# Kernel optimization log

Hardware: AMD Instinct MI355X
Metric: run time of the kernel (lower is better)

Reference implementation:

```python
import jax, jax.numpy as jnp
import numpy as np

T, N, E = 4, 20000, 320000
F_IN, EH, NH, GH, OUT = 12, 32, 64, 64, 1
NUM_LAYERS = 2
EB_IN = (EH + 2 * NH) * 2 + GH  # 384
NB_IN = 2 * NH + 2 * EH + GH    # 256
GB_IN = NH + EH + GH            # 160


def setup_inputs() -> dict:
    key = jax.random.key(0)
    ks = jax.random.split(key, 24)
    f32 = jnp.float32
    def w(k, fan_in, shape):
        return jax.random.normal(k, shape, f32) * (1.0 / np.sqrt(fan_in))
    return {
        "node_attr": jax.random.normal(ks[0], (T, N, F_IN), f32),
        "edge_attr": jax.random.normal(ks[1], (T, E, 1), f32),
        "edge_index": jax.random.randint(ks[2], (2, E), 0, N, jnp.int32),
        "sp_L_vals": jax.random.normal(ks[3], (E,), f32),
        "global_attr": jax.random.normal(ks[4], (1, GH), f32),
        "coeff": jnp.full((1,), 0.1, f32),
        "W_ee": w(ks[5], 1, (1, EH)), "b_ee": jnp.zeros((EH,), f32),
        "W_ne": w(ks[6], F_IN, (F_IN, NH)), "b_ne": jnp.zeros((NH,), f32),
        "W_eb": w(ks[7], EB_IN, (EB_IN, EH)), "b_eb": jnp.zeros((EH,), f32),
        "W_nb": w(ks[8], NB_IN, (NB_IN, NH)), "b_nb": jnp.zeros((NH,), f32),
        "W_gb": w(ks[9], GB_IN, (GB_IN, GH)), "b_gb": jnp.zeros((GH,), f32),
        "W_nd1": w(ks[10], NH, (NH, NH)), "b_nd1": jnp.zeros((NH,), f32),
        "W_nd2": w(ks[11], NH, (NH, OUT)), "b_nd2": jnp.zeros((OUT,), f32),
    }


def _forward(node_attr, edge_attr, edge_index, sp_L_vals, global_attr, coeff,
             W_ee, b_ee, W_ne, b_ne, W_eb, b_eb, W_nb, b_nb, W_gb, b_gb,
             W_nd1, b_nd1, W_nd2, b_nd2):
    relu = jax.nn.relu
    s, r = edge_index[0], edge_index[1]
    seg = lambda v, idx: jax.ops.segment_sum(v, idx, num_segments=N)
    c = coeff[0]

    # encoders
    x_enc = relu(node_attr @ W_ne + b_ne)   # [T,N,NH]
    e_enc = relu(edge_attr @ W_ee + b_ee)   # [T,E,EH]

    def run_gn(xT, eT, g0):
        # recurrent GN core over processing steps; hidden (h_x,h_e,h_g) starts at zeros
        def step(carry, inp):
            h_x, h_e, h_g = carry
            x_in, e_in = inp
            gE = jnp.broadcast_to(h_g, (E, GH))
            # EdgeBlock: [edge_in, edge_h, sender_in, sender_h, recv_in, recv_h, global]
            edge_cat = jnp.concatenate(
                [e_in, h_e, x_in[s], h_x[s], x_in[r], h_x[r], gE], axis=-1)
            e_new = relu(edge_cat @ W_eb + b_eb)              # [E,EH]
            sent = seg(e_new, s)                              # scatter_add by sender
            recv = seg(e_new, r)                              # scatter_add by receiver
            gN = jnp.broadcast_to(h_g, (N, GH))
            node_cat = jnp.concatenate([x_in, h_x, sent, recv, gN], axis=-1)
            x_new = relu(node_cat @ W_nb + b_nb)              # [N,NH]
            # GlobalBlock: scatter_mean == plain mean (single graph)
            g_cat = jnp.concatenate(
                [x_new.mean(0, keepdims=True), e_new.mean(0, keepdims=True), h_g], axis=-1)
            g_new = relu(g_cat @ W_gb + b_gb)                 # [1,GH]
            # physics terms (pde='diff'): time derivative = state update,
            # spatial derivative = coeff * (graph-Laplacian action via sp_L edge weights)
            t_der = x_new - h_x
            s_der = c * seg(sp_L_vals[:, None] * (x_new[s] - x_new[r]), r)
            return (x_new, e_new, g_new), (x_new, e_new, g_new, t_der, s_der)
        carry0 = (jnp.zeros((N, NH), jnp.float32), jnp.zeros((E, EH), jnp.float32), g0)
        _, ys = jax.lax.scan(step, carry0, (xT, eT))
        return ys  # xs[T,N,NH], es[T,E,EH], gs[T,1,GH], td[T,N,NH], sd[T,N,NH]

    xs, es, gs, td, sd = run_gn(x_enc, e_enc, global_attr)
    x_pre = x_enc
    for _ in range(NUM_LAYERS - 1):
        x_res = xs + x_pre          # residual node state feeds next GN layer
        x_pre = x_res
        xs, es, gs, td, sd = run_gn(x_res, es, gs[0])

    x_final = xs + x_pre            # add_residual=True final residual
    h = relu(x_final @ W_nd1 + b_nd1)
    out_nodes = h @ W_nd2 + b_nd2   # [T,N,OUT]
    return out_nodes, td, sd


def reference(node_attr, edge_attr, edge_index, sp_L_vals, global_attr, coeff,
              W_ee, b_ee, W_ne, b_ne, W_eb, b_eb, W_nb, b_nb, W_gb, b_gb,
              W_nd1, b_nd1, W_nd2, b_nd2):
    return _forward(node_attr, edge_attr, edge_index, sp_L_vals, global_attr, coeff,
                    W_ee, b_ee, W_ne, b_ne, W_eb, b_eb, W_nb, b_nb, W_gb, b_gb,
                    W_nd1, b_nd1, W_nd2, b_nd2)
```

## Files before the change

kernel.cpp:

```cpp
#include <hip/hip_runtime.h>


typedef __attribute__((ext_vector_type(8))) short s16x8;
typedef __attribute__((ext_vector_type(4))) float f32x4;

#define T_STEPS 4
#define NN 20000
#define NP 20224
#define NE 320000

__device__ __forceinline__ float bf2f(unsigned short h){
  return __uint_as_float(((unsigned)h)<<16);
}
__device__ __forceinline__ unsigned short f2bf(float f){
  unsigned u = __float_as_uint(f);
  return (unsigned short)((u + 0x7fffu + ((u>>16)&1u)) >> 16);
}
__device__ __forceinline__ float loadIn(const void* p, size_t i, int bf){
  return bf ? bf2f(((const unsigned short*)p)[i]) : ((const float*)p)[i];
}
__device__ __forceinline__ void storeOut(void* o, size_t i, float v, int bf){
  if(bf) ((unsigned short*)o)[i] = f2bf(v);
  else   ((float*)o)[i] = v;
}
__device__ __forceinline__ void load8(const float* __restrict__ p, float* v){
  const float4* q4 = (const float4*)p;
  float4 a = q4[0], b = q4[1];
  v[0]=a.x; v[1]=a.y; v[2]=a.z; v[3]=a.w;
  v[4]=b.x; v[5]=b.y; v[6]=b.z; v[7]=b.w;
}
__device__ __forceinline__ int4 pack8(const float* v){
  unsigned p0 = (unsigned)f2bf(v[0]) | ((unsigned)f2bf(v[1])<<16);
  unsigned p1 = (unsigned)f2bf(v[2]) | ((unsigned)f2bf(v[3])<<16);
  unsigned p2 = (unsigned)f2bf(v[4]) | ((unsigned)f2bf(v[5])<<16);
  unsigned p3 = (unsigned)f2bf(v[6]) | ((unsigned)f2bf(v[7])<<16);
  return make_int4((int)p0,(int)p1,(int)p2,(int)p3);
}
__device__ __forceinline__ void unp8(int4 w, float* a){
  unsigned x;
  x=(unsigned)w.x; a[0]=__uint_as_float(x<<16); a[1]=__uint_as_float(x&0xffff0000u);
  x=(unsigned)w.y; a[2]=__uint_as_float(x<<16); a[3]=__uint_as_float(x&0xffff0000u);
  x=(unsigned)w.z; a[4]=__uint_as_float(x<<16); a[5]=__uint_as_float(x&0xffff0000u);
  x=(unsigned)w.w; a[6]=__uint_as_float(x<<16); a[7]=__uint_as_float(x&0xffff0000u);
}

union I4S8 { int4 i; s16x8 s; };

struct ConvJob { const void* src; float* dst; int n; };
struct ConvJobs { ConvJob j[16]; int cnt; };

__global__ void conv_kernel(ConvJobs jobs, const void* coeff_in, int* flagp,
                            float* coeff_f, float* z, int zn){
  unsigned short u = ((const unsigned short*)coeff_in)[0];
  float as_bf = bf2f(u);
  int bf = (fabsf(as_bf - 0.1f) < 0.02f) ? 1 : 0;
  int tid = blockIdx.x*blockDim.x + threadIdx.x;
  if(tid==0){ *flagp = bf; *coeff_f = bf ? as_bf : ((const float*)coeff_in)[0]; }
  int stride = gridDim.x*blockDim.x;
  for(int q=0;q<jobs.cnt;q++){
    const void* s = jobs.j[q].src; float* d = jobs.j[q].dst; int n = jobs.j[q].n;
    for(int i=tid;i<n;i+=stride) d[i] = loadIn(s, i, bf);
  }
  for(int i=tid;i<zn;i+=stride) z[i]=0.f;
}

__global__ void csr_hist(const int* __restrict__ ei, int* deg_s, int* deg_r,
                         unsigned short* __restrict__ rank_s,
                         unsigned short* __restrict__ rank_r){
  int e = blockIdx.x*256+threadIdx.x;
  rank_s[e] = (unsigned short)atomicAdd(&deg_s[ei[e]],1);
  rank_r[e] = (unsigned short)atomicAdd(&deg_r[ei[NE+e]],1);
}

__global__ void csr_scan(const int* __restrict__ deg_s, int* __restrict__ off_s,
                         const int* __restrict__ deg_r, int* __restrict__ off_r){
  const int CH = NP/256;
  const int* deg = blockIdx.x ? deg_r : deg_s;
  int* off = blockIdx.x ? off_r : off_s;
  int t = threadIdx.x;
  int base = t*CH;
  int s = 0;
  #pragma unroll 8
  for(int i=0;i<CH;i++) s += deg[base+i];
  int lane = t & 63, w = t >> 6;
  int x = s;
  #pragma unroll
  for(int o=1;o<64;o<<=1){
    int y = __shfl_up(x, o, 64);
    if(lane >= o) x += y;
  }
  __shared__ int wtot[4];
  if(lane==63) wtot[w] = x;
  __syncthreads();
  int wbase = 0;
  #pragma unroll
  for(int k=0;k<3;k++) if(k<w) wbase += wtot[k];
  int acc = wbase + x - s;
  #pragma unroll 8
  for(int i=0;i<CH;i++){
    off[base+i]=acc; acc+=deg[base+i];
  }
  if(t==255) off[NN]=acc;
}

__global__ void fill_pack_enc_kernel(
  const int* __restrict__ ei,
  const int* __restrict__ s_off, const int* __restrict__ r_off,
  const unsigned short* __restrict__ rank_s,
  const unsigned short* __restrict__ rank_r,
  int* __restrict__ csr_s, int* __restrict__ csr_r, int2* __restrict__ sr2,
  const void* __restrict__ spL, float* __restrict__ spL_p,
  const void* __restrict__ W_eb_in, const void* __restrict__ W_nb_in,
  const void* __restrict__ W_nd1_in,
  unsigned short* __restrict__ WpE, unsigned short* __restrict__ WpN,
  unsigned short* __restrict__ WpD,
  const void* __restrict__ na, const float* __restrict__ W_ne,
  const float* __restrict__ b_ne, unsigned short* __restrict__ xA,
  const int* flagp)
{
  __shared__ float arow[4][12];
  const int blk = blockIdx.x;
  const int bf = *flagp;
  if(blk < NE/256){
    int e = blk*256+threadIdx.x;
    int s = ei[e], r = ei[NE+e];
    int p = r_off[r] + rank_r[e];
    sr2[p] = make_int2(s,r);
    csr_r[p] = e;
    csr_s[s_off[s]+rank_s[e]] = p;
    spL_p[p] = loadIn(spL, e, bf);
  } else if(blk < NE/256 + 128){
    int idx = (blk - NE/256)*256 + threadIdx.x;
    const void* W; unsigned short* P; int KW, NT;
    if(idx < 12288){ W=W_eb_in; P=WpE; KW=12; NT=2; }
    else if(idx < 28672){ idx -= 12288; W=W_nb_in; P=WpN; KW=8; NT=4; }
    else { idx -= 28672; W=W_nd1_in; P=WpD; KW=2; NT=4; }
    int j = idx & 7;
    int lane = (idx>>3) & 63;
    int rest = idx >> 9;
    int kw = rest % KW;
    int nt = rest / KW;
    int k = kw*32 + (lane>>4)*8 + j;
    int n = nt*16 + (lane&15);
    P[idx] = f2bf(loadIn(W, (size_t)k*(NT*16) + n, bf));
  } else {
    int lane = threadIdx.x & 63, nl = threadIdx.x >> 6;
    int row = (blk - (NE/256 + 128))*4 + nl;
    if(lane<12) arow[nl][lane] = loadIn(na, (size_t)row*12+lane, bf);
    __syncthreads();
    float acc = b_ne[lane];
    #pragma unroll
    for(int k=0;k<12;k++) acc += arow[nl][k]*W_ne[k*64+lane];
    xA[(size_t)row*64+lane] = f2bf(fmaxf(acc,0.f));
  }
}

__global__ __launch_bounds__(256,4) void edge_block_mfma(
  const int2* __restrict__ sr2,
  const unsigned short* __restrict__ x_in,
  const unsigned short* __restrict__ h_x,
  const void* __restrict__ e_attr,
  int e_attr_off,
  const int* __restrict__ inv,
  const unsigned short* __restrict__ e_in,
  const unsigned short* __restrict__ h_e,
  const float* __restrict__ g,
  const float* __restrict__ W_ee, const float* __restrict__ b_ee,
  const unsigned short* __restrict__ Wp,
  const float* __restrict__ b_eb,
  unsigned short* __restrict__ e_out,
  float* __restrict__ partial_e,
  const int* flagp)
{
  const int tid = threadIdx.x;
  const int lane = tid&63;
  const int q = lane>>4, m16 = lane&15;
  const int pair = blockIdx.x*4 + (tid>>6);
  const int e0 = pair*32;
  const int eg0 = e0 + m16, eg1 = e0 + 16 + m16;
  const int2 sr0 = sr2[eg0], sr1 = sr2[eg1];
  const int o8 = q*8;
  const int4 z4 = make_int4(0,0,0,0);

  I4S8 A0[12], A1[12];
  if(e_attr){
    int bf = *flagp;
    float a0v = loadIn(e_attr, (size_t)e_attr_off + inv[eg0], bf);
    float a1v = loadIn(e_attr, (size_t)e_attr_off + inv[eg1], bf);
    float v[8];
    #pragma unroll
    for(int j=0;j<8;j++) v[j] = fmaxf(a0v*W_ee[o8+j]+b_ee[o8+j], 0.f);
    A0[0].i = pack8(v);
    #pragma unroll
    for(int j=0;j<8;j++) v[j] = fmaxf(a1v*W_ee[o8+j]+b_ee[o8+j], 0.f);
    A1[0].i = pack8(v);
  } else {
    A0[0].i = ((const int4*)(e_in + (size_t)eg0*32))[q];
    A1[0].i = ((const int4*)(e_in + (size_t)eg1*32))[q];
  }
  A0[1].i = h_e ? ((const int4*)(h_e + (size_t)eg0*32))[q] : z4;
  A1[1].i = h_e ? ((const int4*)(h_e + (size_t)eg1*32))[q] : z4;
  { const int4* p0 = (const int4*)(x_in + (size_t)sr0.x*64);
    const int4* p1 = (const int4*)(x_in + (size_t)sr1.x*64);
    A0[2].i = p0[q]; A1[2].i = p1[q];
    A0[3].i = p0[4+q]; A1[3].i = p1[4+q]; }
  if(h_x){
    const int4* p0 = (const int4*)(h_x + (size_t)sr0.x*64);
    const int4* p1 = (const int4*)(h_x + (size_t)sr1.x*64);
    A0[4].i = p0[q]; A1[4].i = p1[q];
    A0[5].i = p0[4+q]; A1[5].i = p1[4+q];
  } else { A0[4].i=z4; A1[4].i=z4; A0[5].i=z4; A1[5].i=z4; }
  { const int4* p0 = (const int4*)(x_in + (size_t)sr0.y*64);
    const int4* p1 = (const int4*)(x_in + (size_t)sr1.y*64);
    A0[6].i = p0[q]; A1[6].i = p1[q];
    A0[7].i = p0[4+q]; A1[7].i = p1[4+q]; }
  if(h_x){
    const int4* p0 = (const int4*)(h_x + (size_t)sr0.y*64);
    const int4* p1 = (const int4*)(h_x + (size_t)sr1.y*64);
    A0[8].i = p0[q]; A1[8].i = p1[q];
    A0[9].i = p0[4+q]; A1[9].i = p1[4+q];
  } else { A0[8].i=z4; A1[8].i=z4; A0[9].i=z4; A1[9].i=z4; }
  { float v[8];
    load8(g + o8, v);      A0[10].i = pack8(v); A1[10].i = A0[10].i;
    load8(g + 32 + o8, v); A0[11].i = pack8(v); A1[11].i = A0[11].i; }

  f32x4 a00={0.f,0.f,0.f,0.f}, a01={0.f,0.f,0.f,0.f};
  f32x4 a10={0.f,0.f,0.f,0.f}, a11={0.f,0.f,0.f,0.f};
  #pragma unroll
  for(int kw=0;kw<12;kw++){
    s16x8 b0 = *(const s16x8*)(Wp + (size_t)(kw*64 + lane)*8);
    s16x8 b1 = *(const s16x8*)(Wp + (size_t)((12+kw)*64 + lane)*8);
    a00 = __builtin_amdgcn_mfma_f32_16x16x32_bf16(A0[kw].s, b0, a00, 0,0,0);
    a01 = __builtin_amdgcn_mfma_f32_16x16x32_bf16(A0[kw].s, b1, a01, 0,0,0);
    a10 = __builtin_amdgcn_mfma_f32_16x16x32_bf16(A1[kw].s, b0, a10, 0,0,0);
    a11 = __builtin_amdgcn_mfma_f32_16x16x32_bf16(A1[kw].s, b1, a11, 0,0,0);
  }

  float pe0=0.f, pe1=0.f;
  const float bb0 = b_eb[m16], bb1 = b_eb[16+m16];
  #pragma unroll
  for(int r=0;r<4;r++){
    int eg0m = e0 + q*4 + r;
    int eg1m = eg0m + 16;
    float v00 = fmaxf(a00[r]+bb0, 0.f);
    float v01 = fmaxf(a01[r]+bb1, 0.f);
    float v10 = fmaxf(a10[r]+bb0, 0.f);
    float v11 = fmaxf(a11[r]+bb1, 0.f);
    e_out[(size_t)eg0m*32+m16]    = f2bf(v00);
    e_out[(size_t)eg0m*32+16+m16] = f2bf(v01);
    e_out[(size_t)eg1m*32+m16]    = f2bf(v10);
    e_out[(size_t)eg1m*32+16+m16] = f2bf(v11);
    pe0 += v00+v10; pe1 += v01+v11;
  }
  pe0 += __shfl_xor(pe0,16,64); pe0 += __shfl_xor(pe0,32,64);
  pe1 += __shfl_xor(pe1,16,64); pe1 += __shfl_xor(pe1,32,64);
  if(q==0){
    int slot = blockIdx.x & 63;
    atomicAdd(&partial_e[slot*32+m16],    pe0);
    atomicAdd(&partial_e[slot*32+16+m16], pe1);
  }
}

__global__ void aggregate_kernel(const unsigned short* __restrict__ e_new,
  const int* __restrict__ s_off, const int* __restrict__ csr_s,
  const int* __restrict__ r_off,
  unsigned short* __restrict__ sentB, unsigned short* __restrict__ recvB)
{
  int node = blockIdx.x*4 + (threadIdx.x>>6);
  int lane = threadIdx.x & 63;
  int c4 = (lane & 7) * 4;
  int jr = lane >> 3;
  float s0=0.f,s1=0.f,s2=0.f,s3=0.f;
  float r0=0.f,r1=0.f,r2=0.f,r3=0.f;
  {
    int beg = s_off[node], end = s_off[node+1];
    for(int i=beg+jr; i<end; i+=8){
      uint2 w = *(const uint2*)(e_new + (size_t)csr_s[i]*32 + c4);
      s0 += __uint_as_float(w.x<<16);
      s1 += __uint_as_float(w.x&0xffff0000u);
      s2 += __uint_as_float(w.y<<16);
      s3 += __uint_as_float(w.y&0xffff0000u);
    }
  }
  {
    int beg = r_off[node], end = r_off[node+1];
    for(int i=beg+jr; i<end; i+=8){
      uint2 w = *(const uint2*)(e_new + (size_t)i*32 + c4);
      r0 += __uint_as_float(w.x<<16);
      r1 += __uint_as_float(w.x&0xffff0000u);
      r2 += __uint_as_float(w.y<<16);
      r3 += __uint_as_float(w.y&0xffff0000u);
    }
  }
  #pragma unroll
  for(int o=8;o<64;o<<=1){
    s0 += __shfl_xor(s0,o,64); s1 += __shfl_xor(s1,o,64);
    s2 += __shfl_xor(s2,o,64); s3 += __shfl_xor(s3,o,64);
    r0 += __shfl_xor(r0,o,64); r1 += __shfl_xor(r1,o,64);
    r2 += __shfl_xor(r2,o,64); r3 += __shfl_xor(r3,o,64);
  }
  if(jr==0){
    unsigned slo = (unsigned)f2bf(s0) | ((unsigned)f2bf(s1)<<16);
    unsigned shi = (unsigned)f2bf(s2) | ((unsigned)f2bf(s3)<<16);
    unsigned rlo = (unsigned)f2bf(r0) | ((unsigned)f2bf(r1)<<16);
    unsigned rhi = (unsigned)f2bf(r2) | ((unsigned)f2bf(r3)<<16);
    *(uint2*)(sentB + (size_t)node*32 + c4) = make_uint2(slo,shi);
    *(uint2*)(recvB + (size_t)node*32 + c4) = make_uint2(rlo,rhi);
  }
}

__global__ __launch_bounds__(256) void node_block_mfma(
  const unsigned short* __restrict__ x_in, const unsigned short* __restrict__ h_x,
  const unsigned short* __restrict__ sentB, const unsigned short* __restrict__ recvB,
  const float* __restrict__ g,
  const unsigned short* __restrict__ Wp,
  const float* __restrict__ b_nb,
  unsigned short* __restrict__ x_out,
  unsigned short* __restrict__ xres_out,
  float* __restrict__ partial_x,
  void* __restrict__ out_base, size_t td_off, int has_td,
  float* __restrict__ partial_e,
  const float* __restrict__ W_gb, const float* __restrict__ b_gb,
  float* __restrict__ g_out, int* __restrict__ cnt,
  const int* flagp)
{
  __shared__ int lastFlag;
  __shared__ float gcat[160];
  __shared__ float red[4][64];
  const int tid = threadIdx.x, lane = tid&63;
  const int q = lane>>4, m16 = lane&15;
  const int tile = blockIdx.x*4 + (tid>>6);
  if(tile < NN/16){
    const int n0 = tile*16;
    const int ng = n0+m16;
    const int o8 = q*8;
    const int4 z4 = make_int4(0,0,0,0);

    I4S8 A[8];
    { const int4* xp = (const int4*)(x_in + (size_t)ng*64);
      A[0].i = xp[q]; A[1].i = xp[4+q]; }
    if(h_x){ const int4* hp = (const int4*)(h_x + (size_t)ng*64);
      A[2].i = hp[q]; A[3].i = hp[4+q];
    } else { A[2].i = z4; A[3].i = z4; }
    A[4].i = ((const int4*)(sentB + (size_t)ng*32))[q];
    A[5].i = ((const int4*)(recvB + (size_t)ng*32))[q];
    { float v[8];
      load8(g + o8, v);      A[6].i = pack8(v);
      load8(g + 32 + o8, v); A[7].i = pack8(v); }

    f32x4 acc[4];
    #pragma unroll
    for(int nt=0;nt<4;nt++) acc[nt] = (f32x4){0.f,0.f,0.f,0.f};
    #pragma unroll
    for(int kw=0;kw<8;kw++){
      #pragma unroll
      for(int nt=0;nt<4;nt++){
        s16x8 b = *(const s16x8*)(Wp + (size_t)((nt*8+kw)*64 + lane)*8);
        acc[nt] = __builtin_amdgcn_mfma_f32_16x16x32_bf16(A[kw].s, b, acc[nt], 0,0,0);
      }
    }

    int bf = has_td ? *flagp : 0;
    float ps[4] = {0.f,0.f,0.f,0.f};
    #pragma unroll
    for(int r=0;r<4;r++){
      int nodeg = n0 + q*4 + r;
      #pragma unroll
      for(int nt=0;nt<4;nt++){
        int col = nt*16 + m16;
        float vv = fmaxf(acc[nt][r] + b_nb[col], 0.f);
        unsigned short hb = f2bf(vv);
        x_out[(size_t)nodeg*64+col] = hb;
        if(xres_out){
          float xv = bf2f(x_in[(size_t)nodeg*64+col]);
          xres_out[(size_t)nodeg*64+col] = f2bf(xv + bf2f(hb));
        }
        if(has_td){
          float hxv = h_x ? bf2f(h_x[(size_t)nodeg*64+col]) : 0.f;
          storeOut(out_base, td_off + (size_t)nodeg*64+col, vv - hxv, bf);
        }
        ps[nt] += vv;
      }
    }
    #pragma unroll
    for(int nt=0;nt<4;nt++){
      ps[nt] += __shfl_xor(ps[nt],16,64);
      ps[nt] += __shfl_xor(ps[nt],32,64);
    }
    if(q==0){
      int slot = blockIdx.x & 63;
      #pragma unroll
      for(int nt=0;nt<4;nt++)
        atomicAdd(&partial_x[slot*64 + nt*16 + m16], ps[nt]);
    }
  }

  asm volatile("s_waitcnt vmcnt(0)" ::: "memory");
  __syncthreads();
  if(tid==0) lastFlag = (atomicAdd(cnt,1) == (int)gridDim.x - 1) ? 1 : 0;
  __syncthreads();
  if(!lastFlag) return;

  if(tid<64){
    float sx = 0.f;
    #pragma unroll 8
    for(int i=0;i<64;i++)
      sx += __hip_atomic_load(&partial_x[i*64+tid], __ATOMIC_RELAXED, __HIP_MEMORY_SCOPE_AGENT);
    gcat[tid] = sx * (1.0f/(float)NN);
  } else if(tid<96){
    int j = tid-64;
    float se = 0.f;
    #pragma unroll 8
    for(int i=0;i<64;i++)
      se += __hip_atomic_load(&partial_e[i*32+j], __ATOMIC_RELAXED, __HIP_MEMORY_SCOPE_AGENT);
    gcat[64+j] = se * (1.0f/(float)NE);
  } else if(tid<160){
    gcat[tid] = g[tid-96];
  }
  __syncthreads();
  int j = tid&63, cc = tid>>6;
  float acc2 = 0.f;
  #pragma unroll 8
  for(int k=cc*40;k<cc*40+40;k++) acc2 += gcat[k]*W_gb[k*64+j];
  red[cc][j] = acc2;
  __syncthreads();
  for(int i=tid;i<2048;i+=256) partial_e[i]=0.f;
  for(int i=tid;i<4096;i+=256) partial_x[i]=0.f;
  if(tid<64){
    float a = red[0][tid]+red[1][tid]+red[2][tid]+red[3][tid] + b_gb[tid];
    g_out[tid] = fmaxf(a, 0.f);
  }
  if(tid==0) *cnt = 0;
}

__global__ void sder_csr_kernel(const int2* __restrict__ sr2,
  const float* __restrict__ spL_p, const unsigned short* __restrict__ x_new,
  const int* __restrict__ r_off,
  const float* __restrict__ coeff, void* __restrict__ out_base, size_t off,
  const int* flagp)
{
  int bf = *flagp;
  int lane = threadIdx.x&63, nl = threadIdx.x>>6;
  int node = blockIdx.x*4+nl;
  float xn = bf2f(x_new[(size_t)node*64+lane]);
  float a0=0.f, a1=0.f, a2=0.f, a3=0.f;
  int beg = r_off[node], end = r_off[node+1];
  int i = beg;
  for(; i+4<=end; i+=4){
    float w1 = spL_p[i],   w2 = spL_p[i+1];
    float w3 = spL_p[i+2], w4 = spL_p[i+3];
    int s1 = sr2[i].x, s2 = sr2[i+1].x, s3 = sr2[i+2].x, s4 = sr2[i+3].x;
    a0 += w1*(bf2f(x_new[(size_t)s1*64+lane])-xn);
    a1 += w2*(bf2f(x_new[(size_t)s2*64+lane])-xn);
    a2 += w3*(bf2f(x_new[(size_t)s3*64+lane])-xn);
    a3 += w4*(bf2f(x_new[(size_t)s4*64+lane])-xn);
  }
  for(; i<end; i++){
    float w1 = spL_p[i];
    a0 += w1*(bf2f(x_new[(size_t)sr2[i].x*64+lane])-xn);
  }
  storeOut(out_base, off + (size_t)node*64+lane, coeff[0]*((a0+a1)+(a2+a3)), bf);
}

__global__ __launch_bounds__(256) void decoder_kernel(
  const unsigned short* __restrict__ xs, const unsigned short* __restrict__ xr,
  const unsigned short* __restrict__ WpD,
  const float* __restrict__ b1, const float* __restrict__ W2,
  const float* __restrict__ b2,
  void* __restrict__ out_base, const int* flagp)
{
  const int tid=threadIdx.x, lane=tid&63;
  const int q=lane>>4, m16=lane&15;
  const int tile = blockIdx.x*4 + (tid>>6);
  const int row0 = tile*16;
  const int rg = row0 + m16;

  I4S8 A[2];
  #pragma unroll
  for(int kw=0;kw<2;kw++){
    int4 xa = ((const int4*)(xs + (size_t)rg*64 + kw*32))[q];
    int4 xb = ((const int4*)(xr + (size_t)rg*64 + kw*32))[q];
    float va[8], vb[8], v[8];
    unp8(xa, va); unp8(xb, vb);
    #pragma unroll
    for(int j=0;j<8;j++) v[j] = va[j]+vb[j];
    A[kw].i = pack8(v);
  }

  f32x4 acc[4];
  #pragma unroll
  for(int nt=0;nt<4;nt++) acc[nt] = (f32x4){0.f,0.f,0.f,0.f};
  #pragma unroll
  for(int kw=0;kw<2;kw++){
    #pragma unroll
    for(int nt=0;nt<4;nt++){
      s16x8 b = *(const s16x8*)(WpD + (size_t)((nt*2+kw)*64 + lane)*8);
      acc[nt] = __builtin_amdgcn_mfma_f32_16x16x32_bf16(A[kw].s, b, acc[nt], 0,0,0);
    }
  }

  float val[4];
  #pragma unroll
  for(int r=0;r<4;r++){
    float s = 0.f;
    #pragma unroll
    for(int nt=0;nt<4;nt++){
      int col = nt*16 + m16;
      s += fmaxf(acc[nt][r] + b1[col], 0.f) * W2[col];
    }
    val[r] = s;
  }
  #pragma unroll
  for(int o=1;o<16;o<<=1){
    #pragma unroll
    for(int r=0;r<4;r++) val[r] += __shfl_xor(val[r], o, 64);
  }
  if(m16==0){
    int bf = *flagp;
    float bb = b2[0];
    #pragma unroll
    for(int r=0;r<4;r++)
      storeOut(out_base, (size_t)(row0 + q*4 + r), val[r] + bb, bf);
  }
}

extern "C" void kernel_launch(void* const* d_in, const int* in_sizes, int n_in,
                              void* d_out, int out_size, void* d_ws, size_t ws_size,
                              hipStream_t stream){
  const void* node_attr = d_in[0];
  const void* edge_attr = d_in[1];
  const int*  ei        = (const int*)d_in[2];
  const void* spL       = d_in[3];
  const void* gattr     = d_in[4];
  const void* coeff_in  = d_in[5];
  const void* W_ee_in = d_in[6];  const void* b_ee_in = d_in[7];
  const void* W_ne_in = d_in[8];  const void* b_ne_in = d_in[9];
  const void* W_eb_in = d_in[10]; const void* b_eb_in = d_in[11];
  const void* W_nb_in = d_in[12]; const void* b_nb_in = d_in[13];
  const void* W_gb_in = d_in[14]; const void* b_gb_in = d_in[15];
  const void* W_nd1_in= d_in[16]; const void* b_nd1_in= d_in[17];
  const void* W_nd2_in= d_in[18]; const void* b_nd2_in= d_in[19];

  float* ws = (float*)d_ws;
  float* W_ee_f = ws;             float* b_ee_f = W_ee_f+32;
  float* W_ne_f = b_ee_f+32;      float* b_ne_f = W_ne_f+768;
  float* W_gb_f = b_ne_f+64;      float* b_gb_f = W_gb_f+10240;
  float* W_nd1_f= b_gb_f+64;      float* b_nd1_f= W_nd1_f+4096;
  float* W_nd2_f= b_nd1_f+64;     float* b_nd2_f= W_nd2_f+64;
  float* b_eb_f = b_nd2_f+1;      float* b_nb_f = b_eb_f+32;
  float* coeff_f= b_nb_f+64;
  int*   flagp  = (int*)(ws + 15523);
  float* gbuf   = ws + 15524;
  float* zbase  = ws + 16100;
  int*   cnt    = (int*)zbase;
  float* part_e = zbase + 4;
  float* part_x = part_e + 2048;
  int*   deg_s  = (int*)(part_x + 4096);
  int*   deg_r  = deg_s + NP;
  int*   s_off  = deg_r + NP;
  int*   r_off  = s_off + NP+1;
  unsigned short* rank_s = (unsigned short*)(r_off + NP+1);
  unsigned short* rank_r = rank_s + NE;
  int*   csr_s  = (int*)(rank_r + NE);
  int*   csr_r  = csr_s + NE;
  float* spL_p  = (float*)(csr_r + NE);
  size_t iend   = (size_t)((int*)(spL_p + NE) - (int*)ws);
  iend = (iend + 3) & ~(size_t)3;
  int2*  sr2    = (int2*)(ws + iend);
  unsigned short* sentB = (unsigned short*)(sr2 + NE);
  unsigned short* recvB = sentB + (size_t)NN*32;
  unsigned short* eBuf  = recvB + (size_t)NN*32;
  unsigned short* xA    = eBuf + (size_t)T_STEPS*NE*32;
  unsigned short* xB    = xA + (size_t)T_STEPS*NN*64;
  unsigned short* xC    = xB + (size_t)T_STEPS*NN*64;
  unsigned short* WpE   = xC + (size_t)T_STEPS*NN*64;
  unsigned short* WpN   = WpE + 12288;
  unsigned short* WpD   = WpN + 16384;

  ConvJobs jobs; int c=0;
  auto add=[&](const void* s, float* d, int n){ jobs.j[c].src=s; jobs.j[c].dst=d; jobs.j[c].n=n; c++; };
  add(W_ee_in,W_ee_f,32);   add(b_ee_in,b_ee_f,32);
  add(W_ne_in,W_ne_f,768);  add(b_ne_in,b_ne_f,64);
  add(W_gb_in,W_gb_f,10240);add(b_gb_in,b_gb_f,64);
  add(W_nd1_in,W_nd1_f,4096);add(b_nd1_in,b_nd1_f,64);
  add(W_nd2_in,W_nd2_f,64); add(b_nd2_in,b_nd2_f,1);
  add(b_eb_in,b_eb_f,32);   add(b_nb_in,b_nb_f,64);
  add(gattr,gbuf,64);
  jobs.cnt=c;
  conv_kernel<<<64,256,0,stream>>>(jobs, coeff_in, flagp, coeff_f,
      zbase, 4+2048+4096+2*NP);

  csr_hist<<<NE/256,256,0,stream>>>(ei, deg_s, deg_r, rank_s, rank_r);
  csr_scan<<<2,256,0,stream>>>(deg_s, s_off, deg_r, r_off);

  fill_pack_enc_kernel<<<NE/256 + 128 + T_STEPS*NN/4,256,0,stream>>>(
      ei, s_off, r_off, rank_s, rank_r, csr_s, csr_r, sr2, spL, spL_p,
      W_eb_in, W_nb_in, W_nd1_in, WpE, WpN, WpD,
      node_attr, W_ne_f, b_ne_f, xA, flagp);

  const size_t td_base = (size_t)T_STEPS*NN;
  const size_t sd_base = td_base + (size_t)T_STEPS*NN*64;

  for(int layer=0; layer<2; layer++){
    for(int t=0;t<T_STEPS;t++){
      const unsigned short* x_in = (layer==0? xA : xC) + (size_t)t*NN*64;
      const unsigned short* h_x  = (t>0)? xB + (size_t)(t-1)*NN*64 : nullptr;
      const unsigned short* h_e  = (t>0)? eBuf + (size_t)(t-1)*NE*32 : nullptr;
      const float* gptr = (layer==0)? gbuf + t*64
                                    : (t==0? gbuf+1*64 : gbuf+(4+t)*64);
      float*       gout = (layer==0)? gbuf+(1+t)*64 : gbuf+(5+t)*64;
      const void*  eat  = (layer==0)? edge_attr : nullptr;
      const unsigned short* e_in = (layer==0)? nullptr : eBuf + (size_t)t*NE*32;
      unsigned short*       e_out= eBuf + (size_t)t*NE*32;

      edge_block_mfma<<<NE/128,256,0,stream>>>(sr2, x_in, h_x, eat, t*NE, csr_r,
          e_in, h_e, gptr, W_ee_f, b_ee_f, WpE, b_eb_f, e_out,
          part_e, flagp);

      aggregate_kernel<<<NN/4,256,0,stream>>>(e_out, s_off, csr_s, r_off,
          sentB, recvB);

      unsigned short* x_out = xB + (size_t)t*NN*64;
      unsigned short* xres  = (layer==0)? xC + (size_t)t*NN*64 : nullptr;
      size_t td_off = td_base + (size_t)t*NN*64;
      node_block_mfma<<<(NN/16+3)/4,256,0,stream>>>(x_in, h_x, sentB, recvB, gptr,
          WpN, b_nb_f, x_out, xres, part_x, d_out, td_off, (layer==1)?1:0,
          part_e, W_gb_f, b_gb_f, gout, cnt, flagp);

      if(layer==1){
        sder_csr_kernel<<<NN/4,256,0,stream>>>(sr2, spL_p, x_out, r_off,
            coeff_f, d_out, sd_base + (size_t)t*NN*64, flagp);
      }
    }
  }

  decoder_kernel<<<(T_STEPS*NN/16+3)/4,256,0,stream>>>(xB, xC, WpD,
      b_nd1_f, W_nd2_f, b_nd2_f, d_out, flagp);
}
```

Baseline: 785.3 us.

## Precompute per-node sender/receiver projections before edge block gather

```diff
diff --git a/kernel.cpp b/kernel.cpp
--- a/kernel.cpp
+++ b/kernel.cpp
@@ -113,7 +113,7 @@
   const void* __restrict__ W_eb_in, const void* __restrict__ W_nb_in,
   const void* __restrict__ W_nd1_in,
   unsigned short* __restrict__ WpE, unsigned short* __restrict__ WpN,
-  unsigned short* __restrict__ WpD,
+  unsigned short* __restrict__ WpD, unsigned short* __restrict__ WpP,
   const void* __restrict__ na, const float* __restrict__ W_ne,
   const float* __restrict__ b_ne, unsigned short* __restrict__ xA,
   const int* flagp)
@@ -129,23 +129,35 @@
     csr_r[p] = e;
     csr_s[s_off[s]+rank_s[e]] = p;
     spL_p[p] = loadIn(spL, e, bf);
-  } else if(blk < NE/256 + 128){
+  } else if(blk < NE/256 + 120){
     int idx = (blk - NE/256)*256 + threadIdx.x;
-    const void* W; unsigned short* P; int KW, NT;
-    if(idx < 12288){ W=W_eb_in; P=WpE; KW=12; NT=2; }
-    else if(idx < 28672){ idx -= 12288; W=W_nb_in; P=WpN; KW=8; NT=4; }
-    else { idx -= 28672; W=W_nd1_in; P=WpD; KW=2; NT=4; }
-    int j = idx & 7;
-    int lane = (idx>>3) & 63;
-    int rest = idx >> 9;
-    int kw = rest % KW;
-    int nt = rest / KW;
-    int k = kw*32 + (lane>>4)*8 + j;
-    int n = nt*16 + (lane&15);
-    P[idx] = f2bf(loadIn(W, (size_t)k*(NT*16) + n, bf));
+    if(idx < 22528){
+      const void* W; unsigned short* P; int KW, NT;
+      if(idx < 2048){ W=W_eb_in; P=WpE; KW=2; NT=2; }
+      else if(idx < 18432){ idx -= 2048; W=W_nb_in; P=WpN; KW=8; NT=4; }
+      else { idx -= 18432; W=W_nd1_in; P=WpD; KW=2; NT=4; }
+      int j = idx & 7;
+      int lane = (idx>>3) & 63;
+      int rest = idx >> 9;
+      int kw = rest % KW;
+      int nt = rest / KW;
+      int k = kw*32 + (lane>>4)*8 + j;
+      int n = nt*16 + (lane&15);
+      P[idx] = f2bf(loadIn(W, (size_t)k*(NT*16) + n, bf));
+    } else {
+      int idx2 = idx - 22528;
+      int j = idx2 & 7;
+      int lane = (idx2>>3) & 63;
+      int rest = idx2 >> 9;
+      int kw = rest & 3;
+      int nt = rest >> 2;
+      int row = (nt<2 ? 64 : 192) + kw*32 + (lane>>4)*8 + j;
+      int col = (nt&1)*16 + (lane&15);
+      WpP[idx2] = f2bf(loadIn(W_eb_in, (size_t)row*32 + col, bf));
+    }
   } else {
     int lane = threadIdx.x & 63, nl = threadIdx.x >> 6;
-    int row = (blk - (NE/256 + 128))*4 + nl;
+    int row = (blk - (NE/256 + 120))*4 + nl;
     if(lane<12) arow[nl][lane] = loadIn(na, (size_t)row*12+lane, bf);
     __syncthreads();
     float acc = b_ne[lane];
@@ -155,19 +167,71 @@
   }
 }
 
-__global__ __launch_bounds__(256,4) void edge_block_mfma(
-  const int2* __restrict__ sr2,
+__global__ __launch_bounds__(256) void node_pre_kernel(
   const unsigned short* __restrict__ x_in,
   const unsigned short* __restrict__ h_x,
+  const unsigned short* __restrict__ WpP,
+  const float* __restrict__ g,
+  const void* __restrict__ W_eb_in, const float* __restrict__ b_eb,
+  float* __restrict__ srT, float* __restrict__ gbias,
+  const int* flagp)
+{
+  const int tid = threadIdx.x, lane = tid&63;
+  const int q = lane>>4, m16 = lane&15;
+  if(blockIdx.x >= 313){
+    if(tid < 32){
+      int bf = *flagp;
+      float gb = b_eb[tid];
+      for(int k=0;k<64;k++){
+        float gv = bf2f(f2bf(g[k]));
+        float wv = bf2f(f2bf(loadIn(W_eb_in, (size_t)(320+k)*32 + tid, bf)));
+        gb += gv*wv;
+      }
+      gbias[tid] = gb;
+    }
+    return;
+  }
+  const int tile = blockIdx.x*4 + (tid>>6);
+  if(tile >= NN/16) return;
+  const int n0 = tile*16, ng = n0+m16;
+  const int4 z4 = make_int4(0,0,0,0);
+  I4S8 A[4];
+  { const int4* xp = (const int4*)(x_in + (size_t)ng*64);
+    A[0].i = xp[q]; A[1].i = xp[4+q]; }
+  if(h_x){ const int4* hp = (const int4*)(h_x + (size_t)ng*64);
+    A[2].i = hp[q]; A[3].i = hp[4+q];
+  } else { A[2].i = z4; A[3].i = z4; }
+  f32x4 acc[4];
+  #pragma unroll
+  for(int nt=0;nt<4;nt++) acc[nt] = (f32x4){0.f,0.f,0.f,0.f};
+  #pragma unroll
+  for(int kw=0;kw<4;kw++){
+    #pragma unroll
+    for(int nt=0;nt<4;nt++){
+      s16x8 b = *(const s16x8*)(WpP + (size_t)((nt*4+kw)*64 + lane)*8);
+      acc[nt] = __builtin_amdgcn_mfma_f32_16x16x32_bf16(A[kw].s, b, acc[nt], 0,0,0);
+    }
+  }
+  #pragma unroll
+  for(int r=0;r<4;r++){
+    int n = n0 + q*4 + r;
+    #pragma unroll
+    for(int nt=0;nt<4;nt++)
+      srT[(size_t)n*64 + nt*16 + m16] = acc[nt][r];
+  }
+}
+
+__global__ __launch_bounds__(256) void edge_block_mfma(
+  const int2* __restrict__ sr2,
   const void* __restrict__ e_attr,
   int e_attr_off,
   const int* __restrict__ inv,
   const unsigned short* __restrict__ e_in,
   const unsigned short* __restrict__ h_e,
-  const float* __restrict__ g,
   const float* __restrict__ W_ee, const float* __restrict__ b_ee,
   const unsigned short* __restrict__ Wp,
-  const float* __restrict__ b_eb,
+  const float* __restrict__ srT,
+  const float* __restrict__ gbias,
   unsigned short* __restrict__ e_out,
   float* __restrict__ partial_e,
   const int* flagp)
@@ -178,11 +242,10 @@
   const int pair = blockIdx.x*4 + (tid>>6);
   const int e0 = pair*32;
   const int eg0 = e0 + m16, eg1 = e0 + 16 + m16;
-  const int2 sr0 = sr2[eg0], sr1 = sr2[eg1];
   const int o8 = q*8;
   const int4 z4 = make_int4(0,0,0,0);
 
-  I4S8 A0[12], A1[12];
+  I4S8 A0[2], A1[2];
   if(e_attr){
     int bf = *flagp;
     float a0v = loadIn(e_attr, (size_t)e_attr_off + inv[eg0], bf);
@@ -200,52 +263,44 @@
   }
   A0[1].i = h_e ? ((const int4*)(h_e + (size_t)eg0*32))[q] : z4;
   A1[1].i = h_e ? ((const int4*)(h_e + (size_t)eg1*32))[q] : z4;
-  { const int4* p0 = (const int4*)(x_in + (size_t)sr0.x*64);
-    const int4* p1 = (const int4*)(x_in + (size_t)sr1.x*64);
-    A0[2].i = p0[q]; A1[2].i = p1[q];
-    A0[3].i = p0[4+q]; A1[3].i = p1[4+q]; }
-  if(h_x){
-    const int4* p0 = (const int4*)(h_x + (size_t)sr0.x*64);
-    const int4* p1 = (const int4*)(h_x + (size_t)sr1.x*64);
-    A0[4].i = p0[q]; A1[4].i = p1[q];
-    A0[5].i = p0[4+q]; A1[5].i = p1[4+q];
-  } else { A0[4].i=z4; A1[4].i=z4; A0[5].i=z4; A1[5].i=z4; }
-  { const int4* p0 = (const int4*)(x_in + (size_t)sr0.y*64);
-    const int4* p1 = (const int4*)(x_in + (size_t)sr1.y*64);
-    A0[6].i = p0[q]; A1[6].i = p1[q];
-    A0[7].i = p0[4+q]; A1[7].i = p1[4+q]; }
-  if(h_x){
-    const int4* p0 = (const int4*)(h_x + (size_t)sr0.y*64);
-    const int4* p1 = (const int4*)(h_x + (size_t)sr1.y*64);
-    A0[8].i = p0[q]; A1[8].i = p1[q];
-    A0[9].i = p0[4+q]; A1[9].i = p1[4+q];
-  } else { A0[8].i=z4; A1[8].i=z4; A0[9].i=z4; A1[9].i=z4; }
-  { float v[8];
-    load8(g + o8, v);      A0[10].i = pack8(v); A1[10].i = A0[10].i;
-    load8(g + 32 + o8, v); A0[11].i = pack8(v); A1[11].i = A0[11].i; }
 
   f32x4 a00={0.f,0.f,0.f,0.f}, a01={0.f,0.f,0.f,0.f};
   f32x4 a10={0.f,0.f,0.f,0.f}, a11={0.f,0.f,0.f,0.f};
   #pragma unroll
-  for(int kw=0;kw<12;kw++){
+  for(int kw=0;kw<2;kw++){
     s16x8 b0 = *(const s16x8*)(Wp + (size_t)(kw*64 + lane)*8);
-    s16x8 b1 = *(const s16x8*)(Wp + (size_t)((12+kw)*64 + lane)*8);
+    s16x8 b1 = *(const s16x8*)(Wp + (size_t)((2+kw)*64 + lane)*8);
     a00 = __builtin_amdgcn_mfma_f32_16x16x32_bf16(A0[kw].s, b0, a00, 0,0,0);
     a01 = __builtin_amdgcn_mfma_f32_16x16x32_bf16(A0[kw].s, b1, a01, 0,0,0);
     a10 = __builtin_amdgcn_mfma_f32_16x16x32_bf16(A1[kw].s, b0, a10, 0,0,0);
     a11 = __builtin_amdgcn_mfma_f32_16x16x32_bf16(A1[kw].s, b1, a11, 0,0,0);
   }
 
+  const float gb0 = gbias[m16], gb1 = gbias[16+m16];
+  int2 rw[8];
+  #pragma unroll
+  for(int r=0;r<4;r++){
+    rw[r]   = sr2[e0 + q*4 + r];
+    rw[4+r] = sr2[e0 + 16 + q*4 + r];
+  }
+  float sv0[8], sv1[8], rv0[8], rv1[8];
+  #pragma unroll
+  for(int k=0;k<8;k++){
+    sv0[k] = srT[(size_t)rw[k].x*64 + m16];
+    sv1[k] = srT[(size_t)rw[k].x*64 + 16 + m16];
+    rv0[k] = srT[(size_t)rw[k].y*64 + 32 + m16];
+    rv1[k] = srT[(size_t)rw[k].y*64 + 48 + m16];
+  }
+
   float pe0=0.f, pe1=0.f;
-  const float bb0 = b_eb[m16], bb1 = b_eb[16+m16];
   #pragma unroll
   for(int r=0;r<4;r++){
     int eg0m = e0 + q*4 + r;
     int eg1m = eg0m + 16;
-    float v00 = fmaxf(a00[r]+bb0, 0.f);
-    float v01 = fmaxf(a01[r]+bb1, 0.f);
-    float v10 = fmaxf(a10[r]+bb0, 0.f);
-    float v11 = fmaxf(a11[r]+bb1, 0.f);
+    float v00 = fmaxf(a00[r] + sv0[r]   + rv0[r]   + gb0, 0.f);
+    float v01 = fmaxf(a01[r] + sv1[r]   + rv1[r]   + gb1, 0.f);
+    float v10 = fmaxf(a10[r] + sv0[4+r] + rv0[4+r] + gb0, 0.f);
+    float v11 = fmaxf(a11[r] + sv1[4+r] + rv1[4+r] + gb1, 0.f);
     e_out[(size_t)eg0m*32+m16]    = f2bf(v00);
     e_out[(size_t)eg0m*32+16+m16] = f2bf(v01);
     e_out[(size_t)eg1m*32+m16]    = f2bf(v10);
@@ -574,8 +629,11 @@
   unsigned short* xB    = xA + (size_t)T_STEPS*NN*64;
   unsigned short* xC    = xB + (size_t)T_STEPS*NN*64;
   unsigned short* WpE   = xC + (size_t)T_STEPS*NN*64;
-  unsigned short* WpN   = WpE + 12288;
+  unsigned short* WpN   = WpE + 2048;
   unsigned short* WpD   = WpN + 16384;
+  unsigned short* WpP   = WpD + 4096;
+  float* srT   = (float*)(WpP + 8192);
+  float* gbias = srT + (size_t)NN*64;
 
   ConvJobs jobs; int c=0;
   auto add=[&](const void* s, float* d, int n){ jobs.j[c].src=s; jobs.j[c].dst=d; jobs.j[c].n=n; c++; };
@@ -593,9 +651,9 @@
   csr_hist<<<NE/256,256,0,stream>>>(ei, deg_s, deg_r, rank_s, rank_r);
   csr_scan<<<2,256,0,stream>>>(deg_s, s_off, deg_r, r_off);
 
-  fill_pack_enc_kernel<<<NE/256 + 128 + T_STEPS*NN/4,256,0,stream>>>(
+  fill_pack_enc_kernel<<<NE/256 + 120 + T_STEPS*NN/4,256,0,stream>>>(
       ei, s_off, r_off, rank_s, rank_r, csr_s, csr_r, sr2, spL, spL_p,
-      W_eb_in, W_nb_in, W_nd1_in, WpE, WpN, WpD,
+      W_eb_in, W_nb_in, W_nd1_in, WpE, WpN, WpD, WpP,
       node_attr, W_ne_f, b_ne_f, xA, flagp);
 
   const size_t td_base = (size_t)T_STEPS*NN;
@@ -613,9 +671,11 @@
       const unsigned short* e_in = (layer==0)? nullptr : eBuf + (size_t)t*NE*32;
       unsigned short*       e_out= eBuf + (size_t)t*NE*32;
 
-      edge_block_mfma<<<NE/128,256,0,stream>>>(sr2, x_in, h_x, eat, t*NE, csr_r,
-          e_in, h_e, gptr, W_ee_f, b_ee_f, WpE, b_eb_f, e_out,
-          part_e, flagp);
+      node_pre_kernel<<<314,256,0,stream>>>(x_in, h_x, WpP, gptr,
+          W_eb_in, b_eb_f, srT, gbias, flagp);
+
+      edge_block_mfma<<<NE/128,256,0,stream>>>(sr2, eat, t*NE, csr_r,
+          e_in, h_e, W_ee_f, b_ee_f, WpE, srT, gbias, e_out, part_e, flagp);
 
       aggregate_kernel<<<NN/4,256,0,stream>>>(e_out, s_off, csr_s, r_off,
           sentB, recvB);
```

Result: faster. 764.7 us, median of 2 (-2.6%).
